# Kernel tuning notes

Hardware: AMD Instinct MI355X
Metric: run time of the kernel (lower is better)

Reference implementation:

```python
import jax, jax.numpy as jnp
import numpy as np

EPS = 1e-5
GROUPS = 32

def group_norm(x, gamma, beta):
    B, C, H, W = x.shape
    g = x.reshape(B, GROUPS, C // GROUPS, H, W)
    mu = g.mean(axis=(2, 3, 4), keepdims=True)
    var = g.var(axis=(2, 3, 4), keepdims=True)
    g = (g - mu) * jax.lax.rsqrt(var + EPS)
    x = g.reshape(B, C, H, W)
    return x * gamma[None, :, None, None] + beta[None, :, None, None]

def setup_inputs() -> dict:
    key = jax.random.key(0)
    ks = jax.random.split(key, 6)
    C = 512
    x = jax.random.normal(ks[0], (16, C, 32, 32), dtype=jnp.float32)
    gamma = jnp.ones((C,), jnp.float32)
    beta = jnp.zeros((C,), jnp.float32)
    w_qkv = jax.random.normal(ks[1], (3 * C, C), jnp.float32) / np.sqrt(C)
    b_qkv = jnp.zeros((3 * C,), jnp.float32)
    w_proj = jax.random.normal(ks[2], (C, C), jnp.float32) / np.sqrt(C)
    b_proj = jnp.zeros((C,), jnp.float32)
    return {"x": x, "gamma": gamma, "beta": beta, "w_qkv": w_qkv,
            "b_qkv": b_qkv, "w_proj": w_proj, "b_proj": b_proj}

def reference(x, gamma, beta, w_qkv, b_qkv, w_proj, b_proj):
    B, C, H, W = x.shape
    h = group_norm(x, gamma, beta)
    # 1x1 conv == per-pixel linear over channels
    qkv = jnp.einsum('bchw,oc->bohw', h, w_qkv) + b_qkv[None, :, None, None]
    q, k, v = jnp.split(qkv, 3, axis=1)
    N = H * W
    q = q.reshape(B, C, N)            # [B,C,N]
    k = k.reshape(B, C, N)
    v = v.reshape(B, C, N)
    attn = jnp.einsum('bci,bcj->bij', q, k) / jnp.sqrt(jnp.float32(C))
    attn = jax.nn.softmax(attn, axis=-1)          # [B,N,N]
    out = jnp.einsum('bij,bcj->bci', attn, v)     # [B,C,N]
    out = out.reshape(B, C, H, W)
    out = jnp.einsum('bchw,oc->bohw', out, w_proj) + b_proj[None, :, None, None]
    return x + out
```

## Files before the change

### kernel.cpp

```cpp
#include <hip/hip_runtime.h>
#include <hip/hip_bf16.h>

#define BATCH 16
#define CH    512
#define NPIX  1024
#define GRP   32
#define CPG   16

typedef __attribute__((ext_vector_type(8))) short bf16x8;
typedef __attribute__((ext_vector_type(4))) float f32x4;

__device__ __forceinline__ ushort f2b(float f) {
    union { float f; unsigned u; } v; v.f = f;
    unsigned u = v.u;
    u += 0x7FFF + ((u >> 16) & 1);
    return (ushort)(u >> 16);
}

#define GLD16(gp, lp) __builtin_amdgcn_global_load_lds( \
    (__attribute__((address_space(1))) void*)(gp), \
    (__attribute__((address_space(3))) void*)(lp), 16, 0, 0)

__global__ __launch_bounds__(256) void convert_weights(
    const float* __restrict__ wq, const float* __restrict__ wp,
    ushort* __restrict__ wq_b, ushort* __restrict__ wp_b,
    float* __restrict__ rowsum) {
    int i = blockIdx.x * 256 + threadIdx.x;
    if (i < 786432) wq_b[i] = f2b(wq[i]);
    else            wp_b[i - 786432] = f2b(wp[i - 786432]);
    if (i < BATCH * NPIX) rowsum[i] = 0.f;
}

__global__ __launch_bounds__(256) void gn_stats(
    const float* __restrict__ x, float* __restrict__ mu, float* __restrict__ rs) {
    int g = blockIdx.x, b = blockIdx.y;
    const float4* p = (const float4*)(x + ((size_t)b * CH + g * CPG) * NPIX);
    float s = 0.f, ss = 0.f;
    for (int i = threadIdx.x; i < 4096; i += 256) {
        float4 v = p[i];
        s  += v.x + v.y + v.z + v.w;
        ss += v.x*v.x + v.y*v.y + v.z*v.z + v.w*v.w;
    }
    for (int o = 1; o < 64; o <<= 1) { s += __shfl_xor(s, o); ss += __shfl_xor(ss, o); }
    __shared__ float as[4], bs[4];
    int w = threadIdx.x >> 6;
    if ((threadIdx.x & 63) == 0) { as[w] = s; bs[w] = ss; }
    __syncthreads();
    if (threadIdx.x == 0) {
        s  = as[0] + as[1] + as[2] + as[3];
        ss = bs[0] + bs[1] + bs[2] + bs[3];
        float m = s * (1.0f / 16384.0f);
        float var = ss * (1.0f / 16384.0f) - m * m;
        mu[b * GRP + g] = m;
        rs[b * GRP + g] = rsqrtf(var + 1e-5f);
    }
}

__global__ __launch_bounds__(256) void gn_norm_t(
    const float* __restrict__ x, const float* __restrict__ mu, const float* __restrict__ rs,
    const float* __restrict__ gamma, const float* __restrict__ beta, ushort* __restrict__ hT) {
    int c0 = blockIdx.x * 32, n0 = blockIdx.y * 128, b = blockIdx.z;
    __shared__ ushort t[128 * 32];
    int tid = threadIdx.x;
#pragma unroll
    for (int i = 0; i < 4; i++) {
        int f = tid + i * 256;
        int c = f >> 5, nf = f & 31;
        int cg = c0 + c;
        float m = mu[b * GRP + (cg >> 4)], r = rs[b * GRP + (cg >> 4)];
        float ga = gamma[cg] * r;
        float be = beta[cg] - m * ga;
        float4 v = *(const float4*)(x + ((size_t)(b * CH + cg)) * NPIX + n0 + nf * 4);
        float vv[4] = {v.x, v.y, v.z, v.w};
#pragma unroll
        for (int j = 0; j < 4; j++) {
            int n = nf * 4 + j;
            int pos = (c >> 3) ^ ((n >> 2) & 3);
            t[n * 32 + pos * 8 + (c & 7)] = f2b(vv[j] * ga + be);
        }
    }
    __syncthreads();
#pragma unroll
    for (int i = 0; i < 2; i++) {
        int ch = tid + i * 256;
        int n = ch >> 2, g = ch & 3;
        int pos = g ^ ((n >> 2) & 3);
        uint4 val = *(const uint4*)&t[n * 32 + pos * 8];
        *(uint4*)(hT + ((size_t)b * NPIX + n0 + n) * CH + c0 + g * 8) = val;
    }
}

#define BM 128
#define BN 128
#define BK 64

template<int EPI>
__global__ __launch_bounds__(256, 4) void gemm_bt(
    const ushort* __restrict__ A, long sA, int lda,
    const ushort* __restrict__ Bt, long sB, int ldb,
    int M, int N, int K,
    void* __restrict__ Out, long sO, int ldo,
    const float* __restrict__ bias,
    const float* __restrict__ resid,
    ushort* __restrict__ vout,
    float* __restrict__ rowsum,
    float scale) {
    __shared__ __align__(16) ushort As[BM * BK];
    __shared__ __align__(16) ushort Bs[BN * BK];
    int b = blockIdx.z;
    A  += (size_t)b * sA;
    Bt += (size_t)b * sB;
    int m0 = blockIdx.y * BM, n0 = blockIdx.x * BN;
    int tid = threadIdx.x;
    int lane = tid & 63;
    int wave = tid >> 6;
    int q = lane >> 4, l = lane & 15;
    int wm = (wave >> 1) * 64, wn = (wave & 1) * 64;

    int aoff[4], boff[4];
    ushort* lA[4]; ushort* lB[4];
#pragma unroll
    for (int i = 0; i < 4; i++) {
        int p = tid + i * 256, r = p >> 3, g = (p & 7) ^ (r & 7);
        aoff[i] = (m0 + r) * lda + g * 8;
        boff[i] = (n0 + r) * ldb + g * 8;
        lA[i] = As + p * 8;
        lB[i] = Bs + p * 8;
    }

    int offA[4][2], offB[4][2];
#pragma unroll
    for (int mi = 0; mi < 4; mi++) {
        int r = wm + mi * 16 + l;
#pragma unroll
        for (int kk = 0; kk < 2; kk++)
            offA[mi][kk] = r * 64 + ((((kk << 2) | q) ^ (r & 7)) * 8);
    }
#pragma unroll
    for (int ni = 0; ni < 4; ni++) {
        int r = wn + ni * 16 + l;
#pragma unroll
        for (int kk = 0; kk < 2; kk++)
            offB[ni][kk] = r * 64 + ((((kk << 2) | q) ^ (r & 7)) * 8);
    }

    f32x4 zero = {0.f, 0.f, 0.f, 0.f};
    f32x4 acc[4][4];
#pragma unroll
    for (int mi = 0; mi < 4; mi++)
#pragma unroll
        for (int ni = 0; ni < 4; ni++) acc[mi][ni] = zero;

    for (int k0 = 0; k0 < K; k0 += BK) {
        __syncthreads();
#pragma unroll
        for (int i = 0; i < 4; i++) GLD16(A + aoff[i] + k0, lA[i]);
#pragma unroll
        for (int i = 0; i < 4; i++) GLD16(Bt + boff[i] + k0, lB[i]);
        __syncthreads();
#pragma unroll
        for (int kk = 0; kk < 2; kk++) {
            bf16x8 af[4], bfr[4];
#pragma unroll
            for (int mi = 0; mi < 4; mi++) af[mi]  = *(const bf16x8*)(As + offA[mi][kk]);
#pragma unroll
            for (int ni = 0; ni < 4; ni++) bfr[ni] = *(const bf16x8*)(Bs + offB[ni][kk]);
#pragma unroll
            for (int mi = 0; mi < 4; mi++)
#pragma unroll
                for (int ni = 0; ni < 4; ni++)
                    acc[mi][ni] = __builtin_amdgcn_mfma_f32_16x16x32_bf16(
                        af[mi], bfr[ni], acc[mi][ni], 0, 0, 0);
        }
    }

    if (EPI == 1) {
#pragma unroll
        for (int mi = 0; mi < 4; mi++) {
            float rsum[4] = {0.f, 0.f, 0.f, 0.f};
#pragma unroll
            for (int ni = 0; ni < 4; ni++) {
                int n = n0 + wn + ni * 16 + l;
#pragma unroll
                for (int rg = 0; rg < 4; rg++) {
                    int m = m0 + wm + mi * 16 + q * 4 + rg;
                    float u = __expf(acc[mi][ni][rg] * scale);
                    rsum[rg] += u;
                    ((ushort*)Out)[(size_t)b * sO + (size_t)m * ldo + n] = f2b(u);
                }
            }
#pragma unroll
            for (int rg = 0; rg < 4; rg++) {
                float s = rsum[rg];
                s += __shfl_xor(s, 1); s += __shfl_xor(s, 2);
                s += __shfl_xor(s, 4); s += __shfl_xor(s, 8);
                if (l == 0)
                    atomicAdd(&rowsum[b * NPIX + m0 + wm + mi * 16 + q * 4 + rg], s);
            }
        }
        return;
    }
#pragma unroll
    for (int mi = 0; mi < 4; mi++) {
        float inv[4];
        if (EPI == 2) {
#pragma unroll
            for (int rg = 0; rg < 4; rg++)
                inv[rg] = 1.0f / rowsum[b * NPIX + m0 + wm + mi * 16 + q * 4 + rg];
        }
#pragma unroll
        for (int ni = 0; ni < 4; ni++) {
            int mbase = m0 + wm + mi * 16 + q * 4;
            int n = n0 + wn + ni * 16 + l;
#pragma unroll
            for (int rg = 0; rg < 4; rg++) {
                int m = mbase + rg;
                float v = acc[mi][ni][rg];
                if (EPI == 0) {
                    v += bias[n];
                    if (n < 1024)
                        ((ushort*)Out)[(size_t)b * sO + (size_t)m * ldo + n] = f2b(v);
                    else
                        vout[(size_t)b * (512 * 1024) + (size_t)(n - 1024) * 1024 + m] = f2b(v);
                } else if (EPI == 2) {
                    ((ushort*)Out)[(size_t)b * sO + (size_t)m * ldo + n] = f2b(v * inv[rg]);
                } else {
                    v += bias[m] + resid[(size_t)b * sO + (size_t)m * ldo + n];
                    ((float*)Out)[(size_t)b * sO + (size_t)m * ldo + n] = v;
                }
            }
        }
    }
}

extern "C" void kernel_launch(void* const* d_in, const int* in_sizes, int n_in,
                              void* d_out, int out_size, void* d_ws, size_t ws_size,
                              hipStream_t stream) {
    const float* x     = (const float*)d_in[0];
    const float* gamma = (const float*)d_in[1];
    const float* beta  = (const float*)d_in[2];
    const float* wqkv  = (const float*)d_in[3];
    const float* bqkv  = (const float*)d_in[4];
    const float* wproj = (const float*)d_in[5];
    const float* bproj = (const float*)d_in[6];
    float* out = (float*)d_out;
    char* ws = (char*)d_ws;

    ushort* wq_b   = (ushort*)(ws + 0);
    ushort* wp_b   = (ushort*)(ws + 1572864);
    float*  mu     = (float*)(ws + 2097152);
    float*  rs     = (float*)(ws + 2099200);
    float*  rowsum = (float*)(ws + 2101248);
    ushort* hT     = (ushort*)(ws + 2166784);
    ushort* qk     = (ushort*)(ws + 18944000);
    ushort* vb     = (ushort*)(ws + 52498432);
    ushort* u      = (ushort*)(ws + 69275648);
    ushort* O1T    = hT;

    convert_weights<<<4096, 256, 0, stream>>>(wqkv, wproj, wq_b, wp_b, rowsum);
    gn_stats<<<dim3(GRP, BATCH), 256, 0, stream>>>(x, mu, rs);
    gn_norm_t<<<dim3(16, 8, BATCH), 256, 0, stream>>>(x, mu, rs, gamma, beta, hT);

    gemm_bt<0><<<dim3(12, 8, BATCH), 256, 0, stream>>>(
        hT, 524288, 512, wq_b, 0, 512, 1024, 1536, 512,
        qk, 1048576, 1024, bqkv, nullptr, vb, nullptr, 0.f);

    gemm_bt<1><<<dim3(8, 8, BATCH), 256, 0, stream>>>(
        qk, 1048576, 1024, qk + 512, 1048576, 1024, 1024, 1024, 512,
        u, 1048576, 1024, nullptr, nullptr, nullptr, rowsum, 0.044194173824159216f);

    gemm_bt<2><<<dim3(4, 8, BATCH), 256, 0, stream>>>(
        u, 1048576, 1024, vb, 524288, 1024, 1024, 512, 1024,
        O1T, 524288, 512, nullptr, nullptr, nullptr, rowsum, 0.f);

    gemm_bt<3><<<dim3(8, 4, BATCH), 256, 0, stream>>>(
        wp_b, 0, 512, O1T, 524288, 512, 512, 1024, 512,
        out, 524288, 1024, bproj, x, nullptr, nullptr, 0.f);
}
```

Measured before the change: 247.9 us.

## Double-buffer LDS tiles in GEMM to overlap global loads with MFMA compute

The bf16 GEMM kernel now keeps two LDS buffers per operand. It issues the global-to-LDS loads for the next K tile before computing on the current one, and drops one of the two barriers per K iteration. The aim is to hide global memory latency behind the matrix-core work. In exchange, LDS per block doubles to 64 KB and launch bounds drop from 4 to 2 blocks, which lowers occupancy but leaves more registers per thread. If the compiler adds conservative waits on the async LDS loads before the LDS reads, the overlap may be lost.

```diff
diff --git a/kernel.cpp b/kernel.cpp
--- a/kernel.cpp
+++ b/kernel.cpp
@@ -93,9 +93,11 @@
 #define BM 128
 #define BN 128
 #define BK 64
+#define ABUF (BM * BK)
+#define BBUF (BN * BK)
 
 template<int EPI>
-__global__ __launch_bounds__(256, 4) void gemm_bt(
+__global__ __launch_bounds__(256, 2) void gemm_bt(
     const ushort* __restrict__ A, long sA, int lda,
     const ushort* __restrict__ Bt, long sB, int ldb,
     int M, int N, int K,
@@ -105,8 +107,8 @@
     ushort* __restrict__ vout,
     float* __restrict__ rowsum,
     float scale) {
-    __shared__ __align__(16) ushort As[BM * BK];
-    __shared__ __align__(16) ushort Bs[BN * BK];
+    __shared__ __align__(16) ushort As[2 * ABUF];
+    __shared__ __align__(16) ushort Bs[2 * BBUF];
     int b = blockIdx.z;
     A  += (size_t)b * sA;
     Bt += (size_t)b * sB;
@@ -117,15 +119,13 @@
     int q = lane >> 4, l = lane & 15;
     int wm = (wave >> 1) * 64, wn = (wave & 1) * 64;
 
-    int aoff[4], boff[4];
-    ushort* lA[4]; ushort* lB[4];
+    int aoff[4], boff[4], lof[4];
 #pragma unroll
     for (int i = 0; i < 4; i++) {
         int p = tid + i * 256, r = p >> 3, g = (p & 7) ^ (r & 7);
         aoff[i] = (m0 + r) * lda + g * 8;
         boff[i] = (n0 + r) * ldb + g * 8;
-        lA[i] = As + p * 8;
-        lB[i] = Bs + p * 8;
+        lof[i] = p * 8;
     }
 
     int offA[4][2], offB[4][2];
@@ -151,20 +151,30 @@
 #pragma unroll
         for (int ni = 0; ni < 4; ni++) acc[mi][ni] = zero;
 
+#pragma unroll
+    for (int i = 0; i < 4; i++) GLD16(A + aoff[i], As + lof[i]);
+#pragma unroll
+    for (int i = 0; i < 4; i++) GLD16(Bt + boff[i], Bs + lof[i]);
+
+    int nb = 0;
     for (int k0 = 0; k0 < K; k0 += BK) {
         __syncthreads();
-#pragma unroll
-        for (int i = 0; i < 4; i++) GLD16(A + aoff[i] + k0, lA[i]);
-#pragma unroll
-        for (int i = 0; i < 4; i++) GLD16(Bt + boff[i] + k0, lB[i]);
-        __syncthreads();
+        if (k0 + BK < K) {
+            int xb = (nb ^ 1);
+#pragma unroll
+            for (int i = 0; i < 4; i++) GLD16(A + aoff[i] + k0 + BK, As + xb * ABUF + lof[i]);
+#pragma unroll
+            for (int i = 0; i < 4; i++) GLD16(Bt + boff[i] + k0 + BK, Bs + xb * BBUF + lof[i]);
+        }
+        const ushort* Ab = As + nb * ABUF;
+        const ushort* Bb = Bs + nb * BBUF;
 #pragma unroll
         for (int kk = 0; kk < 2; kk++) {
             bf16x8 af[4], bfr[4];
 #pragma unroll
-            for (int mi = 0; mi < 4; mi++) af[mi]  = *(const bf16x8*)(As + offA[mi][kk]);
-#pragma unroll
-            for (int ni = 0; ni < 4; ni++) bfr[ni] = *(const bf16x8*)(Bs + offB[ni][kk]);
+            for (int mi = 0; mi < 4; mi++) af[mi]  = *(const bf16x8*)(Ab + offA[mi][kk]);
+#pragma unroll
+            for (int ni = 0; ni < 4; ni++) bfr[ni] = *(const bf16x8*)(Bb + offB[ni][kk]);
 #pragma unroll
             for (int mi = 0; mi < 4; mi++)
 #pragma unroll
@@ -172,6 +182,7 @@
                     acc[mi][ni] = __builtin_amdgcn_mfma_f32_16x16x32_bf16(
                         af[mi], bfr[ni], acc[mi][ni], 0, 0, 0);
         }
+        nb ^= 1;
     }
 
     if (EPI == 1) {
```

New measurement: 254.3 us. 1.03x slower.
